# Optimization experiments

Measured on AMD Instinct MI355X. Metric: run time of the kernel, lower is better.

## Reference

```python
import jax, jax.numpy as jnp
import numpy as np

N_NODES = 10000
N_EDGES = 160000
D = 512            # input_dim = hidden_size = output_dim
NUM_EXPERTS = 4
N_LAYERS = 2


def setup_inputs() -> dict:
    key = jax.random.key(0)
    k = jax.random.split(key, 7)
    x = jax.random.normal(k[0], (N_NODES, D), dtype=jnp.float32)
    edge_index = jax.random.randint(k[1], (2, N_EDGES), 0, N_NODES, dtype=jnp.int32)
    # Gating network (Linear D -> NUM_EXPERTS)
    gate_w = jax.random.normal(k[2], (D, NUM_EXPERTS), dtype=jnp.float32) * 0.05
    gate_b = jnp.zeros((NUM_EXPERTS,), dtype=jnp.float32)
    # Per-expert SAGEConv weights: lin_r (self/root) and lin_l (neighbor) + bias
    w_self = jax.random.normal(k[3], (NUM_EXPERTS, N_LAYERS, D, D), dtype=jnp.float32) * 0.05
    w_neigh = jax.random.normal(k[4], (NUM_EXPERTS, N_LAYERS, D, D), dtype=jnp.float32) * 0.05
    b_exp = jnp.zeros((NUM_EXPERTS, N_LAYERS, D), dtype=jnp.float32)
    return {"x": x, "edge_index": edge_index, "gate_w": gate_w, "gate_b": gate_b,
            "w_self": w_self, "w_neigh": w_neigh, "b_exp": b_exp, "top_k": 1}


def reference(x, edge_index, gate_w, gate_b, w_self, w_neigh, b_exp, top_k):
    n = x.shape[0]
    src, dst = edge_index[0], edge_index[1]
    # mean-aggregation normalization (PyG SAGEConv aggr='mean'); 0 for isolated nodes
    deg = jax.ops.segment_sum(jnp.ones_like(src, dtype=x.dtype), dst, num_segments=n)
    inv_deg = jnp.where(deg > 0, 1.0 / jnp.maximum(deg, 1.0), 0.0)[:, None]  # [N,1]

    # gating: softmax(Linear(x)) then top-k routing
    gate = jax.nn.softmax(x @ gate_w + gate_b, axis=-1)          # [N, E]
    top_vals, top_idx = jax.lax.top_k(gate, top_k)               # [N, k]

    def expert(ws, wn, b):  # ws, wn: [L, D, D]; b: [L, D]
        h = x
        for l in range(N_LAYERS):
            agg = jax.ops.segment_sum(h[src], dst, num_segments=n) * inv_deg
            # SAGEConv: lin_l(mean_neigh) + lin_r(x) + bias, then relu (norm='id', eval dropout)
            h = jax.nn.relu(agg @ wn[l] + h @ ws[l] + b[l])
        return h

    # dense all-expert compute (matches original module)
    outs = jax.vmap(expert)(w_self, w_neigh, b_exp)              # [E, N, D]
    outs = jnp.transpose(outs, (1, 0, 2))                        # [N, E, D]
    sel = jnp.take_along_axis(outs, top_idx[:, :, None], axis=1)  # [N, k, D]
    return jnp.sum(sel * top_vals[:, :, None], axis=1)           # [N, D]
```

## Files before the change

kernel.cpp:

```cpp
#include <hip/hip_runtime.h>
#include <hip/hip_bf16.h>
#include <cstdint>

#define N_NODES 10000
#define N_EDGES 160000
#define DIM 512
#define K1 1024
#define NEXP 4

typedef __bf16 bf16_t;
typedef bf16_t bf16x8 __attribute__((ext_vector_type(8)));
typedef float f32x4 __attribute__((ext_vector_type(4)));

#define AS1(p) ((__attribute__((address_space(1))) void*)(p))
#define AS3(p) ((__attribute__((address_space(3))) void*)(p))

#define VMW(N) asm volatile("s_waitcnt vmcnt(" #N ")" ::: "memory")
#define MFMA16(d, a_, b_) d = __builtin_amdgcn_mfma_f32_16x16x32_bf16(a_, b_, d, 0, 0, 0)

__global__ void zero_kernel(int* __restrict__ deg, int* __restrict__ ecnt) {
    int i = blockIdx.x * blockDim.x + threadIdx.x;
    if (i < N_NODES) deg[i] = 0;
    if (i < NEXP) ecnt[i] = 0;
}

__global__ void gate_kernel(const float* __restrict__ x,
                            const float* __restrict__ gw,
                            const float* __restrict__ gb,
                            int* __restrict__ top_idx,
                            float* __restrict__ top_val,
                            bf16_t* __restrict__ acat) {
    const int wave = threadIdx.x >> 6;
    const int lane = threadIdx.x & 63;
    const int node = blockIdx.x * 4 + wave;
    if (node >= N_NODES) return;
    const float4* x4 = (const float4*)(x + (size_t)node * DIM);
    const float4* gw4 = (const float4*)gw;
    float4 xa = x4[lane * 2];
    float4 xb = x4[lane * 2 + 1];
    float xv[8] = { xa.x, xa.y, xa.z, xa.w, xb.x, xb.y, xb.z, xb.w };
    float a0 = 0.f, a1 = 0.f, a2 = 0.f, a3 = 0.f;
    #pragma unroll
    for (int c = 0; c < 8; c++) {
        float4 g = gw4[lane * 8 + c];
        a0 += xv[c] * g.x; a1 += xv[c] * g.y; a2 += xv[c] * g.z; a3 += xv[c] * g.w;
    }
    bf16x8 o;
    #pragma unroll
    for (int c = 0; c < 8; c++) o[c] = (bf16_t)xv[c];
    *(bf16x8*)(acat + (size_t)node * K1 + DIM + lane * 8) = o;
    for (int off = 32; off > 0; off >>= 1) {
        a0 += __shfl_xor(a0, off);
        a1 += __shfl_xor(a1, off);
        a2 += __shfl_xor(a2, off);
        a3 += __shfl_xor(a3, off);
    }
    if (lane == 0) {
        float z[4] = { a0 + gb[0], a1 + gb[1], a2 + gb[2], a3 + gb[3] };
        int bi = 0; float bm = z[0];
        for (int e = 1; e < 4; e++) if (z[e] > bm) { bm = z[e]; bi = e; }
        float den = 0.f;
        for (int e = 0; e < 4; e++) den += expf(z[e] - bm);
        top_idx[node] = bi;
        top_val[node] = 1.0f / den;
    }
}

__global__ void bucket_kernel(const int* __restrict__ top_idx,
                              int* __restrict__ ecnt,
                              int* __restrict__ lists) {
    __shared__ int lcnt[NEXP];
    __shared__ int base[NEXP];
    const int tid = threadIdx.x;
    if (tid < NEXP) lcnt[tid] = 0;
    __syncthreads();
    const int node = blockIdx.x * 256 + tid;
    int e = 0, rank = 0;
    if (node < N_NODES) {
        e = top_idx[node];
        rank = atomicAdd(&lcnt[e], 1);
    }
    __syncthreads();
    if (tid < NEXP) base[tid] = atomicAdd(&ecnt[tid], lcnt[tid]);
    __syncthreads();
    if (node < N_NODES) lists[e * N_NODES + base[e] + rank] = node;
}

__global__ void jobs_kernel(const int* __restrict__ ecnt, int* __restrict__ jobs) {
    if (threadIdx.x == 0 && blockIdx.x == 0) {
        int pref = 0;
        for (int e = 0; e < NEXP; e++) {
            jobs[e] = pref;
            pref += (ecnt[e] + 127) >> 7;
        }
        jobs[4] = pref;
    }
}

__global__ void deg_kernel(const int* __restrict__ dst, int* __restrict__ deg) {
    int i = blockIdx.x * blockDim.x + threadIdx.x;
    if (i < N_EDGES) atomicAdd(&deg[dst[i]], 1);
}

__global__ void scan_kernel(const int* __restrict__ deg,
                            int* __restrict__ offs,
                            int* __restrict__ cursor) {
    __shared__ int wsum[16];
    __shared__ int carrysh;
    const int tid = threadIdx.x;
    const int lane = tid & 63;
    const int wv = tid >> 6;
    if (tid == 0) carrysh = 0;
    __syncthreads();
    for (int base = 0; base < N_NODES; base += 1024) {
        int i = base + tid;
        int v = (i < N_NODES) ? deg[i] : 0;
        int s = v;
        #pragma unroll
        for (int off = 1; off < 64; off <<= 1) {
            int t = __shfl_up(s, off);
            if (lane >= off) s += t;
        }
        if (lane == 63) wsum[wv] = s;
        int carry = carrysh;
        __syncthreads();
        if (wv == 0) {
            int w = (lane < 16) ? wsum[lane] : 0;
            #pragma unroll
            for (int off = 1; off < 16; off <<= 1) {
                int t = __shfl_up(w, off);
                if (lane >= off) w += t;
            }
            if (lane < 16) wsum[lane] = w;
        }
        __syncthreads();
        int wbase = (wv > 0) ? wsum[wv - 1] : 0;
        int excl = carry + wbase + s - v;
        if (i < N_NODES) { offs[i] = excl; cursor[i] = excl; }
        int total = wsum[15];
        __syncthreads();
        if (tid == 0) carrysh = carry + total;
        __syncthreads();
    }
    if (tid == 0) offs[N_NODES] = carrysh;
}

__global__ void fill_kernel(const int* __restrict__ src, const int* __restrict__ dst,
                            int* __restrict__ cursor, int* __restrict__ csr) {
    int i = blockIdx.x * blockDim.x + threadIdx.x;
    if (i < N_EDGES) {
        int d = dst[i];
        int p = atomicAdd(&cursor[d], 1);
        csr[p] = src[i];
    }
}

__global__ void wtrans_kernel(const float* __restrict__ w_neigh,
                              const float* __restrict__ w_self,
                              bf16_t* __restrict__ Bt) {
    __shared__ float tile[32][33];
    const int m = blockIdx.z;
    const bool isSelf = m >= 8;
    const int el = m & 7;
    const float* W = (isSelf ? w_self : w_neigh) + (size_t)el * DIM * DIM;
    const int k0 = blockIdx.x * 32;
    const int n0 = blockIdx.y * 32;
    const int tx = threadIdx.x, ty = threadIdx.y;
    for (int r = ty; r < 32; r += 8)
        tile[r][tx] = W[(size_t)(k0 + r) * DIM + n0 + tx];
    __syncthreads();
    for (int r = ty; r < 32; r += 8) {
        int n = n0 + r;
        int k = k0 + tx;
        Bt[((size_t)el * DIM + n) * K1 + (isSelf ? DIM : 0) + k] = (bf16_t)tile[tx][r];
    }
}

__global__ void agg1_kernel(const int* __restrict__ offs, const int* __restrict__ csr,
                            bf16_t* __restrict__ acat) {
    const int wave = threadIdx.x >> 6;
    const int lane = threadIdx.x & 63;
    const int node = blockIdx.x * 4 + wave;
    if (node >= N_NODES) return;
    const int c0 = lane * 8;
    float s[8] = {0,0,0,0,0,0,0,0};
    int beg = offs[node];
    int end = offs[node + 1];
    int d = end - beg;
    int p = beg;
    for (; p + 8 <= end; p += 8) {
        bf16x8 v[8];
        #pragma unroll
        for (int q = 0; q < 8; q++) {
            int idx = csr[p + q];
            v[q] = *(const bf16x8*)(acat + (size_t)idx * K1 + DIM + c0);
        }
        #pragma unroll
        for (int q = 0; q < 8; q++)
            #pragma unroll
            for (int k = 0; k < 8; k++) s[k] += (float)v[q][k];
    }
    for (; p + 4 <= end; p += 4) {
        bf16x8 v[4];
        #pragma unroll
        for (int q = 0; q < 4; q++) {
            int idx = csr[p + q];
            v[q] = *(const bf16x8*)(acat + (size_t)idx * K1 + DIM + c0);
        }
        #pragma unroll
        for (int q = 0; q < 4; q++)
            #pragma unroll
            for (int k = 0; k < 8; k++) s[k] += (float)v[q][k];
    }
    for (; p < end; p++) {
        int idx = csr[p];
        bf16x8 v0 = *(const bf16x8*)(acat + (size_t)idx * K1 + DIM + c0);
        #pragma unroll
        for (int k = 0; k < 8; k++) s[k] += (float)v0[k];
    }
    float w = d > 0 ? 1.0f / (float)d : 0.0f;
    bf16x8 o;
    #pragma unroll
    for (int k = 0; k < 8; k++) o[k] = (bf16_t)(s[k] * w);
    *(bf16x8*)(acat + (size_t)node * K1 + c0) = o;
}

__global__ void agg2_kernel(const int* __restrict__ offs, const int* __restrict__ csr,
                            const int* __restrict__ top_idx,
                            const bf16_t* __restrict__ h1, bf16_t* __restrict__ acat) {
    const int wave = threadIdx.x >> 6;
    const int lane = threadIdx.x & 63;
    const int node = blockIdx.x * 4 + wave;
    if (node >= N_NODES) return;
    const int c0 = lane * 8;
    const bf16_t* hb = h1 + (size_t)top_idx[node] * N_NODES * DIM;
    float s[8] = {0,0,0,0,0,0,0,0};
    int beg = offs[node];
    int end = offs[node + 1];
    int d = end - beg;
    int p = beg;
    for (; p + 8 <= end; p += 8) {
        bf16x8 v[8];
        #pragma unroll
        for (int q = 0; q < 8; q++) {
            int idx = csr[p + q];
            v[q] = *(const bf16x8*)(hb + (size_t)idx * DIM + c0);
        }
        #pragma unroll
        for (int q = 0; q < 8; q++)
            #pragma unroll
            for (int k = 0; k < 8; k++) s[k] += (float)v[q][k];
    }
    for (; p + 4 <= end; p += 4) {
        bf16x8 v[4];
        #pragma unroll
        for (int q = 0; q < 4; q++) {
            int idx = csr[p + q];
            v[q] = *(const bf16x8*)(hb + (size_t)idx * DIM + c0);
        }
        #pragma unroll
        for (int q = 0; q < 4; q++)
            #pragma unroll
            for (int k = 0; k < 8; k++) s[k] += (float)v[q][k];
    }
    for (; p < end; p++) {
        int idx = csr[p];
        bf16x8 v0 = *(const bf16x8*)(hb + (size_t)idx * DIM + c0);
        #pragma unroll
        for (int k = 0; k < 8; k++) s[k] += (float)v0[k];
    }
    float w = d > 0 ? 1.0f / (float)d : 0.0f;
    bf16x8 o;
    #pragma unroll
    for (int k = 0; k < 8; k++) o[k] = (bf16_t)(s[k] * w);
    *(bf16x8*)(acat + (size_t)node * K1 + c0) = o;
    *(bf16x8*)(acat + (size_t)node * K1 + DIM + c0) = *(const bf16x8*)(hb + (size_t)node * DIM + c0);
}

__global__ __launch_bounds__(512, 2)
void gemm_l1_kernel(const bf16_t* __restrict__ A,
                    const bf16_t* __restrict__ Bt,
                    const float* __restrict__ bias_all,
                    bf16_t* __restrict__ h1) {
    const int b = blockIdx.x;
    const int xcd = b & 7;
    const int loc = b >> 3;
    const int mtile = xcd * 2 + (loc >> 4);
    const int ntile = loc & 15;
    const int e = ntile >> 2;

    __shared__ __align__(16) bf16_t As[3 * 640 * 32];
    __shared__ __align__(16) bf16_t Bs[3 * 128 * 32];

    const int t = threadIdx.x;
    const int lane = t & 63;
    const int wave = t >> 6;
    const int rloc = t >> 2;
    const int cgl = ((t & 3) - ((t >> 3) & 3)) & 3;

    const bf16_t* pA0 = A + (size_t)min(mtile * 640 +   0 + rloc, N_NODES - 1) * K1 + cgl * 8;
    const bf16_t* pA1 = A + (size_t)min(mtile * 640 + 128 + rloc, N_NODES - 1) * K1 + cgl * 8;
    const bf16_t* pA2 = A + (size_t)min(mtile * 640 + 256 + rloc, N_NODES - 1) * K1 + cgl * 8;
    const bf16_t* pA3 = A + (size_t)min(mtile * 640 + 384 + rloc, N_NODES - 1) * K1 + cgl * 8;
    const bf16_t* pA4 = A + (size_t)min(mtile * 640 + 512 + rloc, N_NODES - 1) * K1 + cgl * 8;
    const bf16_t* pB0 = Bt + ((size_t)(e * 2 + 0) * DIM + (ntile & 3) * 128 + rloc) * K1 + cgl * 8;

    char* asb = (char*)&As[0];
    char* bsb = (char*)&Bs[0];

    auto stage_full = [&](int bu) {
        char* ab = asb + bu * 40960 + wave * 1024;
        char* bb = bsb + bu * 8192  + wave * 1024;
        __builtin_amdgcn_global_load_lds(AS1(pA0), AS3(ab),          16, 0, 0);
        __builtin_amdgcn_global_load_lds(AS1(pA1), AS3(ab + 8192),   16, 0, 0);
        __builtin_amdgcn_global_load_lds(AS1(pA2), AS3(ab + 16384),  16, 0, 0);
        __builtin_amdgcn_global_load_lds(AS1(pA3), AS3(ab + 24576),  16, 0, 0);
        __builtin_amdgcn_global_load_lds(AS1(pA4), AS3(ab + 32768),  16, 0, 0);
        __builtin_amdgcn_global_load_lds(AS1(pB0), AS3(bb),          16, 0, 0);
        pA0 += 32; pA1 += 32; pA2 += 32; pA3 += 32; pA4 += 32; pB0 += 32;
    };

    const int rfr = lane & 15;
    const int cpr = lane >> 4;
    const int wm = wave >> 1;
    const int wn = wave & 1;
    const int arow = wm * 160 + rfr;
    const int brow = wn * 64 + rfr;
    const int ppA = (cpr + (arow >> 1)) & 3;
    const int ppB = (cpr + (brow >> 1)) & 3;
    const int aoff = arow * 32 + ppA * 8;
    const int boff = brow * 32 + ppB * 8;

    f32x4 acc[10][4] = {};

    auto compute_full = [&](int bu) {
        const bf16_t* Ab = As + bu * 20480 + aoff;
        const bf16_t* Bb = Bs + bu * 4096  + boff;
        bf16x8 bfr[4];
        #pragma unroll
        for (int j = 0; j < 4; j++) bfr[j] = *(const bf16x8*)(Bb + j * 512);
        #pragma unroll
        for (int i = 0; i < 10; i++) {
            bf16x8 af = *(const bf16x8*)(Ab + i * 512);
            #pragma unroll
            for (int j = 0; j < 4; j++)
                MFMA16(acc[i][j], af, bfr[j]);
        }
    };

    stage_full(0);
    stage_full(1);

    int cb = 0, sb = 2;
    for (int tt = 0; tt < 31; ++tt) {
        VMW(6);
        __builtin_amdgcn_s_barrier();
        asm volatile("" ::: "memory");
        const bool st = (tt < 30);
        char* ab = asb + sb * 40960 + wave * 1024;
        char* bb = bsb + sb * 8192  + wave * 1024;
        const bf16_t* Ab = As + cb * 20480 + aoff;
        const bf16_t* Bb = Bs + cb * 4096  + boff;

        bf16x8 bq[4], aq[4];

        #pragma unroll
        for (int j = 0; j < 4; j++) bq[j] = *(const bf16x8*)(Bb + j * 512);
        #pragma unroll
        for (int i = 0; i < 4; i++) aq[i] = *(const bf16x8*)(Ab + i * 512);
        if (st) {
            __builtin_amdgcn_global_load_lds(AS1(pA0), AS3(ab),        16, 0, 0);
            __builtin_amdgcn_global_load_lds(AS1(pA1), AS3(ab + 8192), 16, 0, 0);
        }
        __builtin_amdgcn_s_barrier();
        asm volatile("s_waitcnt lgkmcnt(0)" ::: "memory");
        __builtin_amdgcn_sched_barrier(0);
        __builtin_amdgcn_s_setprio(1);
        #pragma unroll
        for (int i = 0; i < 4; i++)
            #pragma unroll
            for (int j = 0; j < 4; j++)
                MFMA16(acc[i][j], aq[i], bq[j]);
        __builtin_amdgcn_s_setprio(0);
        __builtin_amdgcn_s_barrier();

        #pragma unroll
        for (int i = 0; i < 3; i++) aq[i] = *(const bf16x8*)(Ab + (4 + i) * 512);
        if (st) {
            __builtin_amdgcn_global_load_lds(AS1(pA2), AS3(ab + 16384), 16, 0, 0);
            __builtin_amdgcn_global_load_lds(AS1(pA3), AS3(ab + 24576), 16, 0, 0);
        }
        __builtin_amdgcn_s_barrier();
        asm volatile("s_waitcnt lgkmcnt(0)" ::: "memory");
        __builtin_amdgcn_sched_barrier(0);
        __builtin_amdgcn_s_setprio(1);
        #pragma unroll
        for (int i = 0; i < 3; i++)
            #pragma unroll
            for (int j = 0; j < 4; j++)
                MFMA16(acc[4 + i][j], aq[i], bq[j]);
        __builtin_amdgcn_s_setprio(0);
        __builtin_amdgcn_s_barrier();

        #pragma unroll
        for (int i = 0; i < 3; i++) aq[i] = *(const bf16x8*)(Ab + (7 + i) * 512);
        if (st) {
            __builtin_amdgcn_global_load_lds(AS1(pA4), AS3(ab + 32768), 16, 0, 0);
            __builtin_amdgcn_global_load_lds(AS1(pB0), AS3(bb),         16, 0, 0);
        }
        __builtin_amdgcn_s_barrier();
        asm volatile("s_waitcnt lgkmcnt(0)" ::: "memory");
        __builtin_amdgcn_sched_barrier(0);
        __builtin_amdgcn_s_setprio(1);
        #pragma unroll
        for (int i = 0; i < 3; i++)
            #pragma unroll
            for (int j = 0; j < 4; j++)
                MFMA16(acc[7 + i][j], aq[i], bq[j]);
        __builtin_amdgcn_s_setprio(0);
        __builtin_amdgcn_s_barrier();

        if (st) {
            pA0 += 32; pA1 += 32; pA2 += 32; pA3 += 32; pA4 += 32; pB0 += 32;
            sb = (sb == 2) ? 0 : sb + 1;
        }
        cb = (cb == 2) ? 0 : cb + 1;
    }
    VMW(0);
    __builtin_amdgcn_s_barrier();
    asm volatile("" ::: "memory");
    compute_full(cb);

    const float* bias = bias_all + e * 1024;
    const int cobase = (ntile & 3) * 128 + wn * 64 + (lane & 15);
    float bv[4];
    #pragma unroll
    for (int j = 0; j < 4; j++) bv[j] = bias[cobase + j * 16];
    const int rbase = mtile * 640 + wm * 160 + (lane >> 4) * 4;
    #pragma unroll
    for (int i = 0; i < 10; i++) {
        #pragma unroll
        for (int r = 0; r < 4; r++) {
            int row = rbase + i * 16 + r;
            if (row < N_NODES) {
                bf16_t* cp = h1 + ((size_t)e * N_NODES + row) * DIM + cobase;
                #pragma unroll
                for (int j = 0; j < 4; j++) {
                    float v = fmaxf(acc[i][j][r] + bv[j], 0.f);
                    cp[j * 16] = (bf16_t)v;
                }
            }
        }
    }
}

__global__ __launch_bounds__(256)
void gemm2_kernel(const bf16_t* __restrict__ A,
                  const bf16_t* __restrict__ Bt,
                  const float* __restrict__ bias_all,
                  float* __restrict__ out,
                  const int* __restrict__ lists,
                  const int* __restrict__ ecnt,
                  const int* __restrict__ jobs,
                  const float* __restrict__ top_val) {
    __shared__ __align__(16) bf16_t As[3 * 128 * 32];
    __shared__ __align__(16) bf16_t Bs[3 * 128 * 32];

    const int t = threadIdx.x;
    const int lane = t & 63;
    const int wave = t >> 6;
    const int wm = wave >> 1;
    const int wn = wave & 1;
    const int r0 = t >> 2;
    const int rot = (t >> 3) & 3;
    const int cgl = ((t & 3) - rot) & 3;
    const int cpr = lane >> 4;
    const int rfr = lane & 15;
    char* asb = (char*)&As[0];
    char* bsb = (char*)&Bs[0];
    const int wb = wave * 1024;

    const int total = jobs[4] * 4;

    for (int j = blockIdx.x; j < total; j += gridDim.x) {
        const int byt = j >> 2;
        const int bx = j & 3;
        const int e = (byt >= jobs[1]) + (byt >= jobs[2]) + (byt >= jobs[3]);
        const int by = byt - jobs[e];
        const int cnt = ecnt[e];
        const int cmax = max(cnt, 1);

        int i0 = by * 128 + r0;
        int i1 = i0 + 64;
        int arow0 = lists[e * N_NODES + min(i0, cmax - 1)];
        int arow1 = lists[e * N_NODES + min(i1, cmax - 1)];
        arow0 = min(max(arow0, 0), N_NODES - 1);
        arow1 = min(max(arow1, 0), N_NODES - 1);
        const bf16_t* Bte = Bt + (size_t)(e * 2 + 1) * DIM * K1;
        const bf16_t* aptr0 = A + (size_t)arow0 * K1 + cgl * 8;
        const bf16_t* aptr1 = A + (size_t)arow1 * K1 + cgl * 8;
        const bf16_t* bptr0 = Bte + (size_t)(bx * 128 + r0) * K1 + cgl * 8;
        const bf16_t* bptr1 = bptr0 + (size_t)64 * K1;

        f32x4 acc[4][4] = {};

        auto stage = [&](int bu) {
            char* ab = asb + bu * 8192 + wb;
            char* bb = bsb + bu * 8192 + wb;
            __builtin_amdgcn_global_load_lds(AS1(aptr0), AS3(ab),        16, 0, 0);
            __builtin_amdgcn_global_load_lds(AS1(aptr1), AS3(ab + 4096), 16, 0, 0);
            __builtin_amdgcn_global_load_lds(AS1(bptr0), AS3(bb),        16, 0, 0);
            __builtin_amdgcn_global_load_lds(AS1(bptr1), AS3(bb + 4096), 16, 0, 0);
            aptr0 += 32; aptr1 += 32; bptr0 += 32; bptr1 += 32;
        };

        auto compute = [&](int bu) {
            const bf16_t* Ab = As + bu * 4096;
            const bf16_t* Bb = Bs + bu * 4096;
            bf16x8 af[4], bfr[4];
            #pragma unroll
            for (int i = 0; i < 4; i++) {
                int r_full = wm * 64 + i * 16 + rfr;
                int p = (cpr + (r_full >> 1)) & 3;
                af[i] = *(const bf16x8*)(Ab + r_full * 32 + p * 8);
            }
            #pragma unroll
            for (int jj = 0; jj < 4; jj++) {
                int r_full = wn * 64 + jj * 16 + rfr;
                int p = (cpr + (r_full >> 1)) & 3;
                bfr[jj] = *(const bf16x8*)(Bb + r_full * 32 + p * 8);
            }
            #pragma unroll
            for (int i = 0; i < 4; i++)
                #pragma unroll
                for (int jj = 0; jj < 4; jj++)
                    MFMA16(acc[i][jj], af[i], bfr[jj]);
        };

        __builtin_amdgcn_s_barrier();
        asm volatile("" ::: "memory");

        stage(0);
        stage(1);
        int cb = 0, sb = 2;
        for (int tt = 0; tt < 31; ++tt) {
            VMW(4);
            __builtin_amdgcn_s_barrier();
            asm volatile("" ::: "memory");
            if (tt < 30) {
                stage(sb);
                sb = (sb == 2) ? 0 : sb + 1;
            }
            compute(cb);
            cb = (cb == 2) ? 0 : cb + 1;
        }
        VMW(0);
        __builtin_amdgcn_s_barrier();
        asm volatile("" ::: "memory");
        compute(cb);

        const float* bias = bias_all + e * 1024 + DIM;
        const int cbase = bx * 128 + wn * 64 + (lane & 15);
        float bv[4];
        #pragma unroll
        for (int jj = 0; jj < 4; jj++) bv[jj] = bias[cbase + jj * 16];
        #pragma unroll
        for (int i = 0; i < 4; i++) {
            #pragma unroll
            for (int r = 0; r < 4; r++) {
                int row = by * 128 + wm * 64 + i * 16 + (lane >> 4) * 4 + r;
                if (row < cnt) {
                    int node = lists[e * N_NODES + row];
                    float tv = top_val[node];
                    float* cp = out + (size_t)node * DIM + cbase;
                    #pragma unroll
                    for (int jj = 0; jj < 4; jj++) {
                        float v = fmaxf(acc[i][jj][r] + bv[jj], 0.f);
                        cp[jj * 16] = v * tv;
                    }
                }
            }
        }
    }
}

extern "C" void kernel_launch(void* const* d_in, const int* in_sizes, int n_in,
                              void* d_out, int out_size, void* d_ws, size_t ws_size,
                              hipStream_t stream) {
    const float* x       = (const float*)d_in[0];
    const int*   edge    = (const int*)d_in[1];
    const float* gw      = (const float*)d_in[2];
    const float* gb      = (const float*)d_in[3];
    const float* w_self  = (const float*)d_in[4];
    const float* w_neigh = (const float*)d_in[5];
    const float* b_exp   = (const float*)d_in[6];
    float* out = (float*)d_out;

    char* p = (char*)d_ws;
    auto alloc = [&](size_t bytes) {
        char* r = p;
        p += (bytes + 255) & ~(size_t)255;
        return r;
    };
    bf16_t* Bt      = (bf16_t*)alloc((size_t)8 * DIM * K1 * 2);
    bf16_t* acat    = (bf16_t*)alloc((size_t)N_NODES * K1 * 2);
    bf16_t* h1      = (bf16_t*)alloc((size_t)NEXP * N_NODES * DIM * 2);
    int*    deg     = (int*)alloc((size_t)N_NODES * 4);
    int*    offs    = (int*)alloc((size_t)(N_NODES + 1) * 4);
    int*    cursor  = (int*)alloc((size_t)N_NODES * 4);
    int*    csr     = (int*)alloc((size_t)N_EDGES * 4);
    int*    top_idx = (int*)alloc((size_t)N_NODES * 4);
    float*  top_val = (float*)alloc((size_t)N_NODES * 4);
    int*    ecnt    = (int*)alloc(256);
    int*    lists   = (int*)alloc((size_t)NEXP * N_NODES * 4);
    int*    jobs    = ecnt + 8;

    const int* srcE = edge;
    const int* dstE = edge + N_EDGES;

    zero_kernel<<<40, 256, 0, stream>>>(deg, ecnt);
    gate_kernel<<<N_NODES / 4, 256, 0, stream>>>(x, gw, gb, top_idx, top_val, acat);
    bucket_kernel<<<40, 256, 0, stream>>>(top_idx, ecnt, lists);
    jobs_kernel<<<1, 1, 0, stream>>>(ecnt, jobs);
    deg_kernel<<<N_EDGES / 256, 256, 0, stream>>>(dstE, deg);
    scan_kernel<<<1, 1024, 0, stream>>>(deg, offs, cursor);
    fill_kernel<<<N_EDGES / 256, 256, 0, stream>>>(srcE, dstE, cursor, csr);
    wtrans_kernel<<<dim3(16, 16, 16), dim3(32, 8), 0, stream>>>(w_neigh, w_self, Bt);
    agg1_kernel<<<N_NODES / 4, 256, 0, stream>>>(offs, csr, acat);
    gemm_l1_kernel<<<256, 512, 0, stream>>>(acat, Bt, b_exp, h1);
    agg2_kernel<<<N_NODES / 4, 256, 0, stream>>>(offs, csr, top_idx, h1, acat);
    gemm2_kernel<<<320, 256, 0, stream>>>(acat, Bt, b_exp, out, lists, ecnt, jobs, top_val);
}
```

Before: 273.6 us.

## Fold zero and jobs kernels into neighbors and drop trailing GEMM barriers

Zeroing of deg and ecnt moves into gate_kernel, and the jobs prefix computation moves into scan_kernel, which removes two tiny kernel launches. Separately, the barrier after each MFMA phase in the pipelined GEMM main loop is removed, so only one barrier per phase remains. The fewer launches cut dispatch overhead. Removing barriers lets waves drift apart, which could let a global_load_lds overwrite an LDS buffer that another wave is still reading, a possible correctness risk.

Result: no change. 268.8 us (-1.8%).

```diff
diff --git a/kernel.cpp b/kernel.cpp
--- a/kernel.cpp
+++ b/kernel.cpp
@@ -18,18 +18,18 @@
 #define VMW(N) asm volatile("s_waitcnt vmcnt(" #N ")" ::: "memory")
 #define MFMA16(d, a_, b_) d = __builtin_amdgcn_mfma_f32_16x16x32_bf16(a_, b_, d, 0, 0, 0)
 
-__global__ void zero_kernel(int* __restrict__ deg, int* __restrict__ ecnt) {
-    int i = blockIdx.x * blockDim.x + threadIdx.x;
-    if (i < N_NODES) deg[i] = 0;
-    if (i < NEXP) ecnt[i] = 0;
-}
-
 __global__ void gate_kernel(const float* __restrict__ x,
                             const float* __restrict__ gw,
                             const float* __restrict__ gb,
                             int* __restrict__ top_idx,
                             float* __restrict__ top_val,
-                            bf16_t* __restrict__ acat) {
+                            bf16_t* __restrict__ acat,
+                            int* __restrict__ deg,
+                            int* __restrict__ ecnt) {
+    const int gid = blockIdx.x * 256 + threadIdx.x;
+    if (gid < N_NODES) deg[gid] = 0;
+    if (gid < NEXP) ecnt[gid] = 0;
+
     const int wave = threadIdx.x >> 6;
     const int lane = threadIdx.x & 63;
     const int node = blockIdx.x * 4 + wave;
@@ -86,17 +86,6 @@
     if (node < N_NODES) lists[e * N_NODES + base[e] + rank] = node;
 }
 
-__global__ void jobs_kernel(const int* __restrict__ ecnt, int* __restrict__ jobs) {
-    if (threadIdx.x == 0 && blockIdx.x == 0) {
-        int pref = 0;
-        for (int e = 0; e < NEXP; e++) {
-            jobs[e] = pref;
-            pref += (ecnt[e] + 127) >> 7;
-        }
-        jobs[4] = pref;
-    }
-}
-
 __global__ void deg_kernel(const int* __restrict__ dst, int* __restrict__ deg) {
     int i = blockIdx.x * blockDim.x + threadIdx.x;
     if (i < N_EDGES) atomicAdd(&deg[dst[i]], 1);
@@ -104,13 +93,23 @@
 
 __global__ void scan_kernel(const int* __restrict__ deg,
                             int* __restrict__ offs,
-                            int* __restrict__ cursor) {
+                            int* __restrict__ cursor,
+                            const int* __restrict__ ecnt,
+                            int* __restrict__ jobs) {
     __shared__ int wsum[16];
     __shared__ int carrysh;
     const int tid = threadIdx.x;
     const int lane = tid & 63;
     const int wv = tid >> 6;
-    if (tid == 0) carrysh = 0;
+    if (tid == 0) {
+        carrysh = 0;
+        int pref = 0;
+        for (int e2 = 0; e2 < NEXP; e2++) {
+            jobs[e2] = pref;
+            pref += (ecnt[e2] + 127) >> 7;
+        }
+        jobs[4] = pref;
+    }
     __syncthreads();
     for (int base = 0; base < N_NODES; base += 1024) {
         int i = base + tid;
@@ -382,7 +381,6 @@
             for (int j = 0; j < 4; j++)
                 MFMA16(acc[i][j], aq[i], bq[j]);
         __builtin_amdgcn_s_setprio(0);
-        __builtin_amdgcn_s_barrier();
 
         #pragma unroll
         for (int i = 0; i < 3; i++) aq[i] = *(const bf16x8*)(Ab + (4 + i) * 512);
@@ -400,7 +398,6 @@
             for (int j = 0; j < 4; j++)
                 MFMA16(acc[4 + i][j], aq[i], bq[j]);
         __builtin_amdgcn_s_setprio(0);
-        __builtin_amdgcn_s_barrier();
 
         #pragma unroll
         for (int i = 0; i < 3; i++) aq[i] = *(const bf16x8*)(Ab + (7 + i) * 512);
@@ -418,7 +415,6 @@
             for (int j = 0; j < 4; j++)
                 MFMA16(acc[7 + i][j], aq[i], bq[j]);
         __builtin_amdgcn_s_setprio(0);
-        __builtin_amdgcn_s_barrier();
 
         if (st) {
             pA0 += 32; pA1 += 32; pA2 += 32; pA3 += 32; pA4 += 32; pB0 += 32;
@@ -618,12 +614,10 @@
     const int* srcE = edge;
     const int* dstE = edge + N_EDGES;
 
-    zero_kernel<<<40, 256, 0, stream>>>(deg, ecnt);
-    gate_kernel<<<N_NODES / 4, 256, 0, stream>>>(x, gw, gb, top_idx, top_val, acat);
+    gate_kernel<<<N_NODES / 4, 256, 0, stream>>>(x, gw, gb, top_idx, top_val, acat, deg, ecnt);
     bucket_kernel<<<40, 256, 0, stream>>>(top_idx, ecnt, lists);
-    jobs_kernel<<<1, 1, 0, stream>>>(ecnt, jobs);
     deg_kernel<<<N_EDGES / 256, 256, 0, stream>>>(dstE, deg);
-    scan_kernel<<<1, 1024, 0, stream>>>(deg, offs, cursor);
+    scan_kernel<<<1, 1024, 0, stream>>>(deg, offs, cursor, ecnt, jobs);
     fill_kernel<<<N_EDGES / 256, 256, 0, stream>>>(srcE, dstE, cursor, csr);
     wtrans_kernel<<<dim3(16, 16, 16), dim3(32, 8), 0, stream>>>(w_neigh, w_self, Bt);
     agg1_kernel<<<N_NODES / 4, 256, 0, stream>>>(offs, csr, acat);
```
